# Kernel optimization log

Measured on AMD Instinct MI355X. Metric: run time of the kernel, lower is better.

Reference implementation:

```python
import jax, jax.numpy as jnp
import numpy as np

B, S, HS = 2, 2048, 2048
H, KVH, D = 8, 1, 256
ROPE_BASE = 10000.0


def _rope_cos_sin(position_ids, dim, base=ROPE_BASE):
    # position_ids: (B, S) int -> cos/sin: (B, S, dim)
    inv_freq = 1.0 / (base ** (jnp.arange(0, dim, 2, dtype=jnp.float32) / dim))
    thetas = position_ids.astype(jnp.float32)[..., None] * inv_freq  # (B,S,dim/2)
    emb = jnp.concatenate([thetas, thetas], axis=-1)  # (B,S,dim)
    return jnp.cos(emb), jnp.sin(emb)


def _rotate_half(x):
    x1, x2 = jnp.split(x, 2, axis=-1)
    return jnp.concatenate([-x2, x1], axis=-1)


def _apply_rope(q, k, cos, sin):
    # q,k: (B,h,S,D); cos,sin: (B,S,D) -> unsqueeze head dim
    cos = cos[:, None, :, :]
    sin = sin[:, None, :, :]
    q_emb = q * cos + _rotate_half(q) * sin
    k_emb = k * cos + _rotate_half(k) * sin
    return q_emb, k_emb


def setup_inputs() -> dict:
    key = jax.random.key(0)
    k0, k1, k2, k3, k4 = jax.random.split(key, 5)
    hidden_states = jax.random.normal(k0, (B, S, HS), jnp.float32)
    # causal additive mask: 0 where j<=i, large negative otherwise
    causal = jnp.tril(jnp.ones((S, S), dtype=bool))
    attention_mask = jnp.where(causal, 0.0, -1e9).astype(jnp.float32)
    attention_mask = jnp.broadcast_to(attention_mask[None, None], (B, 1, S, S))
    position_ids = jnp.broadcast_to(jnp.arange(S, dtype=jnp.int32)[None], (B, S))
    scale = 0.02
    Wq = jax.random.normal(k1, (HS, H * D), jnp.float32) * scale
    Wk = jax.random.normal(k2, (HS, KVH * D), jnp.float32) * scale
    Wv = jax.random.normal(k3, (HS, KVH * D), jnp.float32) * scale
    Wo = jax.random.normal(k4, (H * D, HS), jnp.float32) * scale
    return {"hidden_states": hidden_states, "attention_mask": attention_mask,
            "position_ids": position_ids, "Wq": Wq, "Wk": Wk, "Wv": Wv, "Wo": Wo}


def reference(hidden_states, attention_mask, position_ids, Wq, Wk, Wv, Wo):
    bs, seq_len, _ = hidden_states.shape
    q = (hidden_states @ Wq).reshape(bs, seq_len, H, D).transpose(0, 2, 1, 3)     # (B,H,S,D)
    k = (hidden_states @ Wk).reshape(bs, seq_len, KVH, D).transpose(0, 2, 1, 3)   # (B,KVH,S,D)
    v = (hidden_states @ Wv).reshape(bs, seq_len, KVH, D).transpose(0, 2, 1, 3)
    cos, sin = _rope_cos_sin(position_ids, D)
    q, k = _apply_rope(q, k, cos, sin)
    n_rep = H // KVH
    k = jnp.repeat(k, n_rep, axis=1)  # GQA repeat -> (B,H,S,D)
    v = jnp.repeat(v, n_rep, axis=1)
    scores = jnp.einsum('bhqd,bhkd->bhqk', q, k) / jnp.sqrt(jnp.float32(D))
    scores = scores + attention_mask
    attn = jax.nn.softmax(scores.astype(jnp.float32), axis=-1).astype(q.dtype)
    out = jnp.einsum('bhqk,bhkd->bhqd', attn, v)            # (B,H,S,D)
    out = out.transpose(0, 2, 1, 3).reshape(bs, seq_len, H * D)
    return out @ Wo
```

## Files before the change

kernel.cpp:

```cpp
#include <hip/hip_runtime.h>
#include <hip/hip_bf16.h>

typedef __bf16 bf16x8 __attribute__((ext_vector_type(8)));
typedef __bf16 bf16x4 __attribute__((ext_vector_type(4)));
typedef float  f32x4  __attribute__((ext_vector_type(4)));

#define MFMA16(a, b, c) __builtin_amdgcn_mfma_f32_16x16x32_bf16((a), (b), (c), 0, 0, 0)

#define GLOBAL_AS(p) ((const __attribute__((address_space(1))) void*)(p))
#define LDS_AS(p)    ((__attribute__((address_space(3))) void*)(p))

__global__ __launch_bounds__(256) void cvt_bf16_kernel(const float* __restrict__ in,
                                                       __bf16* __restrict__ out)
{
    const int idx = blockIdx.x * 256 + threadIdx.x;
    const float4* p = (const float4*)in + (size_t)idx * 2;
    float4 a = p[0], b = p[1];
    bf16x8 o;
    o[0] = (__bf16)a.x; o[1] = (__bf16)a.y; o[2] = (__bf16)a.z; o[3] = (__bf16)a.w;
    o[4] = (__bf16)b.x; o[5] = (__bf16)b.y; o[6] = (__bf16)b.z; o[7] = (__bf16)b.w;
    ((bf16x8*)out)[idx] = o;
}

__global__ __launch_bounds__(128) void trig_kernel(float2* __restrict__ cs)
{
    const int s = blockIdx.x, i = threadIdx.x;
    const float theta = (float)s * exp2f((float)i * (-13.287712379549449f / 128.f));
    float sn, c;
    sincosf(theta, &sn, &c);
    cs[s * 128 + i] = make_float2(c, sn);
}

__global__ __launch_bounds__(256) void transpose_cvt_kernel(const float* __restrict__ W,
                                                            __bf16* __restrict__ Bt,
                                                            int K, int N)
{
    __shared__ float t[32][33];
    const int n0 = blockIdx.x * 32, k0 = blockIdx.y * 32;
    const int x = threadIdx.x, y = threadIdx.y;
#pragma unroll
    for (int r = 0; r < 4; ++r)
        t[y + r * 8][x] = W[(size_t)(k0 + y + r * 8) * N + n0 + x];
    __syncthreads();
#pragma unroll
    for (int r = 0; r < 4; ++r)
        Bt[(size_t)(n0 + y + r * 8) * K + k0 + x] = (__bf16)t[x][y + r * 8];
}

__global__ __launch_bounds__(256) void vt_kernel(const __bf16* __restrict__ qkv,
                                                 __bf16* __restrict__ vT)
{
    __shared__ __bf16 t[32][33];
    const int s0 = blockIdx.x * 32, d0 = blockIdx.y * 32, b = blockIdx.z;
    const int x = threadIdx.x, y = threadIdx.y;
#pragma unroll
    for (int r = 0; r < 4; ++r)
        t[y + r * 8][x] = qkv[(size_t)(b * 2048 + s0 + y + r * 8) * 2560 + 2304 + d0 + x];
    __syncthreads();
#pragma unroll
    for (int r = 0; r < 4; ++r)
        vT[(size_t)(b * 256 + d0 + y + r * 8) * 2048 + s0 + x] = t[x][y + r * 8];
}

template <typename TC>
__global__ __launch_bounds__(256) void gemm_bt(const __bf16* __restrict__ A,
                                               const __bf16* __restrict__ Bt,
                                               TC* __restrict__ C,
                                               int M, int N, int K)
{
    __shared__ __bf16 As[128 * 32];
    __shared__ __bf16 Bs[128 * 32];

    const int tid  = threadIdx.x;
    const int wave = tid >> 6, lane = tid & 63;
    const int quad = lane >> 4, l16 = lane & 15;
    const int wm = (wave >> 1) * 64, wn = (wave & 1) * 64;
    const int bm = blockIdx.y * 128, bn = blockIdx.x * 128;

    f32x4 acc[4][4] = {};

    for (int k0 = 0; k0 < K; k0 += 32) {
        __syncthreads();
#pragma unroll
        for (int c = 0; c < 2; ++c) {
            const int off = tid * 16 + c * 4096;
            const int row = off >> 6;
            const int kb  = (off & 63) >> 1;
            const __bf16* ga = A  + (size_t)(bm + row) * K + k0 + kb;
            const __bf16* gb = Bt + (size_t)(bn + row) * K + k0 + kb;
            __builtin_amdgcn_global_load_lds(GLOBAL_AS(ga), LDS_AS(As + (off >> 1)), 16, 0, 0);
            __builtin_amdgcn_global_load_lds(GLOBAL_AS(gb), LDS_AS(Bs + (off >> 1)), 16, 0, 0);
        }
        __syncthreads();

        bf16x8 af[4];
#pragma unroll
        for (int mi = 0; mi < 4; ++mi)
            af[mi] = *(const bf16x8*)&As[(wm + mi * 16 + l16) * 32 + quad * 8];
#pragma unroll
        for (int ni = 0; ni < 4; ++ni) {
            bf16x8 bfr = *(const bf16x8*)&Bs[(wn + ni * 16 + l16) * 32 + quad * 8];
#pragma unroll
            for (int mi = 0; mi < 4; ++mi)
                acc[mi][ni] = MFMA16(af[mi], bfr, acc[mi][ni]);
        }
    }
#pragma unroll
    for (int mi = 0; mi < 4; ++mi)
#pragma unroll
        for (int ni = 0; ni < 4; ++ni)
#pragma unroll
            for (int r = 0; r < 4; ++r) {
                int row = bm + wm + mi * 16 + quad * 4 + r;
                int col = bn + wn + ni * 16 + l16;
                C[(size_t)row * N + col] = (TC)acc[mi][ni][r];
            }
}

__global__ __launch_bounds__(256) void rope_kernel(__bf16* __restrict__ qkv,
                                                   const float2* __restrict__ cs)
{
    const int bs = blockIdx.x;
    const int s = bs & 2047;
    const int t = threadIdx.x;
    const float QS = 0.09016843787599907f;

    const int hh = t >> 5, i0 = (t & 31) * 4;
    float2 c0 = cs[s * 128 + i0 + 0], c1 = cs[s * 128 + i0 + 1];
    float2 c2 = cs[s * 128 + i0 + 2], c3 = cs[s * 128 + i0 + 3];

    {
        __bf16* p = qkv + (size_t)bs * 2560 + hh * 256 + i0;
        bf16x4 x1 = *(const bf16x4*)p;
        bf16x4 x2 = *(const bf16x4*)(p + 128);
        bf16x4 o1, o2;
        o1[0] = (__bf16)(((float)x1[0] * c0.x - (float)x2[0] * c0.y) * QS);
        o2[0] = (__bf16)(((float)x2[0] * c0.x + (float)x1[0] * c0.y) * QS);
        o1[1] = (__bf16)(((float)x1[1] * c1.x - (float)x2[1] * c1.y) * QS);
        o2[1] = (__bf16)(((float)x2[1] * c1.x + (float)x1[1] * c1.y) * QS);
        o1[2] = (__bf16)(((float)x1[2] * c2.x - (float)x2[2] * c2.y) * QS);
        o2[2] = (__bf16)(((float)x2[2] * c2.x + (float)x1[2] * c2.y) * QS);
        o1[3] = (__bf16)(((float)x1[3] * c3.x - (float)x2[3] * c3.y) * QS);
        o2[3] = (__bf16)(((float)x2[3] * c3.x + (float)x1[3] * c3.y) * QS);
        *(bf16x4*)p = o1;
        *(bf16x4*)(p + 128) = o2;
    }
    if (t < 32) {
        const int j0 = t * 4;
        float2 d0 = cs[s * 128 + j0 + 0], d1 = cs[s * 128 + j0 + 1];
        float2 d2 = cs[s * 128 + j0 + 2], d3 = cs[s * 128 + j0 + 3];
        __bf16* p = qkv + (size_t)bs * 2560 + 2048 + j0;
        bf16x4 x1 = *(const bf16x4*)p;
        bf16x4 x2 = *(const bf16x4*)(p + 128);
        bf16x4 o1, o2;
        o1[0] = (__bf16)((float)x1[0] * d0.x - (float)x2[0] * d0.y);
        o2[0] = (__bf16)((float)x2[0] * d0.x + (float)x1[0] * d0.y);
        o1[1] = (__bf16)((float)x1[1] * d1.x - (float)x2[1] * d1.y);
        o2[1] = (__bf16)((float)x2[1] * d1.x + (float)x1[1] * d1.y);
        o1[2] = (__bf16)((float)x1[2] * d2.x - (float)x2[2] * d2.y);
        o2[2] = (__bf16)((float)x2[2] * d2.x + (float)x1[2] * d2.y);
        o1[3] = (__bf16)((float)x1[3] * d3.x - (float)x2[3] * d3.y);
        o2[3] = (__bf16)((float)x2[3] * d3.x + (float)x1[3] * d3.y);
        *(bf16x4*)p = o1;
        *(bf16x4*)(p + 128) = o2;
    }
}

__global__ __launch_bounds__(256) void attn_kernel(const __bf16* __restrict__ qkv,
                                                   const __bf16* __restrict__ vTg,
                                                   __bf16* __restrict__ og)
{
    __shared__ __bf16 Ks[64 * 256];
    __shared__ __bf16 Vs[272 * 64];
    __shared__ __bf16 Ps[4][16][68];

    const int b = blockIdx.z, h = blockIdx.y;
    const int qt = (int)gridDim.x - 1 - (int)blockIdx.x;
    const int q0 = qt * 64;
    const int tid  = threadIdx.x;
    const int wave = tid >> 6, lane = tid & 63;
    const int quad = lane >> 4, l16 = lane & 15;
    const int xork = l16 & 7;

    if (tid < 128) {
        bf16x8 one;
#pragma unroll
        for (int e = 0; e < 8; ++e) one[e] = (__bf16)1.0f;
        *(bf16x8*)&Vs[256 * 64 + tid * 8] = one;
    }

    const int qrow = q0 + wave * 16 + l16;
    const __bf16* qptr = qkv + (size_t)(b * 2048 + qrow) * 2560 + h * 256;
    bf16x8 qf[8];
#pragma unroll
    for (int dc = 0; dc < 8; ++dc)
        qf[dc] = *(const bf16x8*)(qptr + dc * 32 + quad * 8);

    f32x4 oacc[17] = {};
    float m_r[4] = {-1e30f, -1e30f, -1e30f, -1e30f};

    const int kKey0 = tid >> 5;
    const int kC    = (tid & 31) ^ (kKey0 & 7);
    const __bf16* kstage0 = qkv + (size_t)b * 2048 * 2560 + 2048
                          + (size_t)kKey0 * 2560 + kC * 8;
    const int vD0 = tid >> 3;
    const int vC  = (tid & 7) ^ (vD0 & 7);
    const __bf16* vstage0 = vTg + (size_t)b * 256 * 2048 + (size_t)vD0 * 2048 + vC * 8;

    int ckK[8];
#pragma unroll
    for (int dc = 0; dc < 8; ++dc) ckK[dc] = (dc * 4 + quad) ^ xork;
    const int chV0 = quad ^ xork;
    const int chV1 = (4 + quad) ^ xork;

    for (int j0 = 0; j0 <= q0; j0 += 64) {
        __syncthreads();
        const __bf16* kst = kstage0 + (size_t)j0 * 2560;
        const __bf16* vst = vstage0 + j0;
#pragma unroll
        for (int p = 0; p < 8; ++p)
            __builtin_amdgcn_global_load_lds(GLOBAL_AS(kst + (size_t)p * 8 * 2560),
                                             LDS_AS(Ks + tid * 8 + p * 2048), 16, 0, 0);
#pragma unroll
        for (int p = 0; p < 8; ++p)
            __builtin_amdgcn_global_load_lds(GLOBAL_AS(vst + (size_t)p * 32 * 2048),
                                             LDS_AS(Vs + tid * 8 + p * 2048), 16, 0, 0);
        __syncthreads();

        f32x4 sc[4] = {};
#pragma unroll
        for (int nt = 0; nt < 4; ++nt) {
            const __bf16* krow = &Ks[(nt * 16 + l16) * 256];
#pragma unroll
            for (int dc = 0; dc < 8; ++dc) {
                bf16x8 kf = *(const bf16x8*)(krow + ckK[dc] * 8);
                sc[nt] = MFMA16(qf[dc], kf, sc[nt]);
            }
        }
        if (j0 == q0) {
#pragma unroll
            for (int nt = 0; nt < 4; ++nt) {
                int key = j0 + nt * 16 + l16;
#pragma unroll
                for (int r = 0; r < 4; ++r) {
                    int row = q0 + wave * 16 + quad * 4 + r;
                    if (key > row) sc[nt][r] = -1e30f;
                }
            }
        }
#pragma unroll
        for (int r = 0; r < 4; ++r) {
            float mx = fmaxf(fmaxf(sc[0][r], sc[1][r]), fmaxf(sc[2][r], sc[3][r]));
#pragma unroll
            for (int off = 1; off < 16; off <<= 1)
                mx = fmaxf(mx, __shfl_xor(mx, off, 64));
            float mnew  = fmaxf(m_r[r], mx);
            float alpha = exp2f(m_r[r] - mnew);
            m_r[r] = mnew;
#pragma unroll
            for (int nt = 0; nt < 4; ++nt)
                sc[nt][r] = exp2f(sc[nt][r] - mnew);
#pragma unroll
            for (int t = 0; t < 17; ++t)
                oacc[t][r] *= alpha;
        }
#pragma unroll
        for (int nt = 0; nt < 4; ++nt)
#pragma unroll
            for (int r = 0; r < 4; ++r)
                Ps[wave][quad * 4 + r][nt * 16 + l16] = (__bf16)sc[nt][r];
        bf16x8 pf0 = *(const bf16x8*)&Ps[wave][l16][quad * 8];
        bf16x8 pf1 = *(const bf16x8*)&Ps[wave][l16][32 + quad * 8];
#pragma unroll
        for (int dt = 0; dt < 17; ++dt) {
            const __bf16* vrow = &Vs[(dt * 16 + l16) * 64];
            bf16x8 vf0 = *(const bf16x8*)(vrow + chV0 * 8);
            bf16x8 vf1 = *(const bf16x8*)(vrow + chV1 * 8);
            oacc[dt] = MFMA16(pf0, vf0, oacc[dt]);
            oacc[dt] = MFMA16(pf1, vf1, oacc[dt]);
        }
    }
    float invl[4];
#pragma unroll
    for (int r = 0; r < 4; ++r) invl[r] = 1.f / oacc[16][r];
#pragma unroll
    for (int dt = 0; dt < 16; ++dt)
#pragma unroll
        for (int r = 0; r < 4; ++r) {
            int row = q0 + wave * 16 + quad * 4 + r;
            int col = h * 256 + dt * 16 + l16;
            og[(size_t)(b * 2048 + row) * 2048 + col] = (__bf16)(oacc[dt][r] * invl[r]);
        }
}

extern "C" void kernel_launch(void* const* d_in, const int* in_sizes, int n_in,
                              void* d_out, int out_size, void* d_ws, size_t ws_size,
                              hipStream_t stream)
{
    (void)in_sizes; (void)n_in; (void)out_size; (void)ws_size;
    const float* hidden = (const float*)d_in[0];
    const float* Wq = (const float*)d_in[3];
    const float* Wk = (const float*)d_in[4];
    const float* Wv = (const float*)d_in[5];
    const float* Wo = (const float*)d_in[6];

    char* ws = (char*)d_ws;
    __bf16* hb    = (__bf16*)(ws);
    __bf16* qkv   = (__bf16*)(ws + (16u << 20));
    __bf16* vTb   = (__bf16*)(ws + (36u << 20));
    __bf16* ob    = (__bf16*)(ws + (38u << 20));
    __bf16* Wqkvt = (__bf16*)(ws + (54u << 20));
    __bf16* Wot   = (__bf16*)(ws + (64u << 20));
    float2* csb   = (float2*)(ws + (72u << 20));
    float* out = (float*)d_out;

    dim3 blk(256);
    dim3 tblk(32, 8);
    cvt_bf16_kernel<<<dim3(4096), blk, 0, stream>>>(hidden, hb);
    trig_kernel<<<dim3(2048), dim3(128), 0, stream>>>(csb);
    transpose_cvt_kernel<<<dim3(64, 64), tblk, 0, stream>>>(Wq, Wqkvt, 2048, 2048);
    transpose_cvt_kernel<<<dim3(8, 64), tblk, 0, stream>>>(Wk, Wqkvt + (size_t)2048 * 2048, 2048, 256);
    transpose_cvt_kernel<<<dim3(8, 64), tblk, 0, stream>>>(Wv, Wqkvt + (size_t)2304 * 2048, 2048, 256);
    transpose_cvt_kernel<<<dim3(64, 64), tblk, 0, stream>>>(Wo, Wot, 2048, 2048);
    gemm_bt<__bf16><<<dim3(20, 32), blk, 0, stream>>>(hb, Wqkvt, qkv, 4096, 2560, 2048);
    rope_kernel<<<dim3(4096), blk, 0, stream>>>(qkv, csb);
    vt_kernel<<<dim3(64, 8, 2), tblk, 0, stream>>>(qkv, vTb);
    attn_kernel<<<dim3(32, 8, 2), blk, 0, stream>>>(qkv, vTb, ob);
    gemm_bt<float><<<dim3(16, 32), blk, 0, stream>>>(ob, Wot, out, 4096, 2048, 2048);
}
```

Measured before the change: 387.7 us.

## Pair low/high causal query tiles per block and double-buffer K/V loads

Each attention block now handles two query tiles (pr and 31-pr), so causal work is balanced across blocks and every loaded K/V tile is used by both query tiles. K/V staging is double-buffered, with the next tile prefetched into LDS while the current one is computed, and one barrier per iteration is removed. The grid is halved to 256 blocks, and register use roughly doubles because two sets of accumulators are held, forcing launch_bounds occupancy to one block. The prefetch into the other buffer is issued right after the barrier and is relied on to complete before the next iteration; that ordering may need explicit waits.

```diff
diff --git a/kernel.cpp b/kernel.cpp
--- a/kernel.cpp
+++ b/kernel.cpp
@@ -166,17 +166,75 @@
     }
 }
 
-__global__ __launch_bounds__(256) void attn_kernel(const __bf16* __restrict__ qkv,
-                                                   const __bf16* __restrict__ vTg,
-                                                   __bf16* __restrict__ og)
-{
-    __shared__ __bf16 Ks[64 * 256];
-    __shared__ __bf16 Vs[272 * 64];
+__device__ __forceinline__ void tile_step(const __bf16* Ksb, const __bf16* Vsb,
+                                          __bf16 (*Psw)[68],
+                                          const bf16x8* qf, f32x4* oacc, float* m_r,
+                                          int rowbase, int keybase, bool diag,
+                                          const int* ckK, int chV0, int chV1,
+                                          int quad, int l16)
+{
+    f32x4 sc[4] = {};
+#pragma unroll
+    for (int nt = 0; nt < 4; ++nt) {
+        const __bf16* krow = Ksb + (nt * 16 + l16) * 256;
+#pragma unroll
+        for (int dc = 0; dc < 8; ++dc) {
+            bf16x8 kf = *(const bf16x8*)(krow + ckK[dc] * 8);
+            sc[nt] = MFMA16(qf[dc], kf, sc[nt]);
+        }
+    }
+    if (diag) {
+#pragma unroll
+        for (int nt = 0; nt < 4; ++nt) {
+            int key = keybase + nt * 16 + l16;
+#pragma unroll
+            for (int r = 0; r < 4; ++r)
+                if (key > rowbase + r) sc[nt][r] = -1e30f;
+        }
+    }
+#pragma unroll
+    for (int r = 0; r < 4; ++r) {
+        float mx = fmaxf(fmaxf(sc[0][r], sc[1][r]), fmaxf(sc[2][r], sc[3][r]));
+#pragma unroll
+        for (int off = 1; off < 16; off <<= 1)
+            mx = fmaxf(mx, __shfl_xor(mx, off, 64));
+        float mnew  = fmaxf(m_r[r], mx);
+        float alpha = exp2f(m_r[r] - mnew);
+        m_r[r] = mnew;
+#pragma unroll
+        for (int nt = 0; nt < 4; ++nt)
+            sc[nt][r] = exp2f(sc[nt][r] - mnew);
+#pragma unroll
+        for (int t = 0; t < 17; ++t)
+            oacc[t][r] *= alpha;
+    }
+#pragma unroll
+    for (int nt = 0; nt < 4; ++nt)
+#pragma unroll
+        for (int r = 0; r < 4; ++r)
+            Psw[quad * 4 + r][nt * 16 + l16] = (__bf16)sc[nt][r];
+    bf16x8 pf0 = *(const bf16x8*)&Psw[l16][quad * 8];
+    bf16x8 pf1 = *(const bf16x8*)&Psw[l16][32 + quad * 8];
+#pragma unroll
+    for (int dt = 0; dt < 17; ++dt) {
+        const __bf16* vrow = Vsb + (dt * 16 + l16) * 64;
+        bf16x8 vf0 = *(const bf16x8*)(vrow + chV0 * 8);
+        bf16x8 vf1 = *(const bf16x8*)(vrow + chV1 * 8);
+        oacc[dt] = MFMA16(pf0, vf0, oacc[dt]);
+        oacc[dt] = MFMA16(pf1, vf1, oacc[dt]);
+    }
+}
+
+__global__ __launch_bounds__(256, 1) void attn_kernel(const __bf16* __restrict__ qkv,
+                                                      const __bf16* __restrict__ vTg,
+                                                      __bf16* __restrict__ og)
+{
+    __shared__ __bf16 Ks[2][64 * 256];
+    __shared__ __bf16 Vs[2][272 * 64];
     __shared__ __bf16 Ps[4][16][68];
 
-    const int b = blockIdx.z, h = blockIdx.y;
-    const int qt = (int)gridDim.x - 1 - (int)blockIdx.x;
-    const int q0 = qt * 64;
+    const int b = blockIdx.z, h = blockIdx.y, pr = blockIdx.x;
+    const int q0L = pr * 64, q0H = (31 - pr) * 64;
     const int tid  = threadIdx.x;
     const int wave = tid >> 6, lane = tid & 63;
     const int quad = lane >> 4, l16 = lane & 15;
@@ -186,18 +244,24 @@
         bf16x8 one;
 #pragma unroll
         for (int e = 0; e < 8; ++e) one[e] = (__bf16)1.0f;
-        *(bf16x8*)&Vs[256 * 64 + tid * 8] = one;
-    }
-
-    const int qrow = q0 + wave * 16 + l16;
-    const __bf16* qptr = qkv + (size_t)(b * 2048 + qrow) * 2560 + h * 256;
-    bf16x8 qf[8];
-#pragma unroll
-    for (int dc = 0; dc < 8; ++dc)
-        qf[dc] = *(const bf16x8*)(qptr + dc * 32 + quad * 8);
-
-    f32x4 oacc[17] = {};
-    float m_r[4] = {-1e30f, -1e30f, -1e30f, -1e30f};
+        *(bf16x8*)&Vs[0][256 * 64 + tid * 8] = one;
+        *(bf16x8*)&Vs[1][256 * 64 + tid * 8] = one;
+    }
+
+    bf16x8 qfL[8], qfH[8];
+    {
+        const __bf16* qpL = qkv + (size_t)(b * 2048 + q0L + wave * 16 + l16) * 2560 + h * 256;
+        const __bf16* qpH = qkv + (size_t)(b * 2048 + q0H + wave * 16 + l16) * 2560 + h * 256;
+#pragma unroll
+        for (int dc = 0; dc < 8; ++dc) {
+            qfL[dc] = *(const bf16x8*)(qpL + dc * 32 + quad * 8);
+            qfH[dc] = *(const bf16x8*)(qpH + dc * 32 + quad * 8);
+        }
+    }
+
+    f32x4 oaccL[17] = {}, oaccH[17] = {};
+    float mL[4] = {-1e30f, -1e30f, -1e30f, -1e30f};
+    float mH[4] = {-1e30f, -1e30f, -1e30f, -1e30f};
 
     const int kKey0 = tid >> 5;
     const int kC    = (tid & 31) ^ (kKey0 & 7);
@@ -213,83 +277,65 @@
     const int chV0 = quad ^ xork;
     const int chV1 = (4 + quad) ^ xork;
 
-    for (int j0 = 0; j0 <= q0; j0 += 64) {
+    const int rowbL = q0L + wave * 16 + quad * 4;
+    const int rowbH = q0H + wave * 16 + quad * 4;
+    const int J = 31 - pr;
+
+    {
+        const __bf16* kst = kstage0;
+        const __bf16* vst = vstage0;
+#pragma unroll
+        for (int p8 = 0; p8 < 8; ++p8)
+            __builtin_amdgcn_global_load_lds(GLOBAL_AS(kst + (size_t)p8 * 8 * 2560),
+                                             LDS_AS(&Ks[0][0] + tid * 8 + p8 * 2048), 16, 0, 0);
+#pragma unroll
+        for (int p8 = 0; p8 < 8; ++p8)
+            __builtin_amdgcn_global_load_lds(GLOBAL_AS(vst + (size_t)p8 * 32 * 2048),
+                                             LDS_AS(&Vs[0][0] + tid * 8 + p8 * 2048), 16, 0, 0);
+    }
+
+    for (int j = 0; j <= J; ++j) {
         __syncthreads();
-        const __bf16* kst = kstage0 + (size_t)j0 * 2560;
-        const __bf16* vst = vstage0 + j0;
-#pragma unroll
-        for (int p = 0; p < 8; ++p)
-            __builtin_amdgcn_global_load_lds(GLOBAL_AS(kst + (size_t)p * 8 * 2560),
-                                             LDS_AS(Ks + tid * 8 + p * 2048), 16, 0, 0);
-#pragma unroll
-        for (int p = 0; p < 8; ++p)
-            __builtin_amdgcn_global_load_lds(GLOBAL_AS(vst + (size_t)p * 32 * 2048),
-                                             LDS_AS(Vs + tid * 8 + p * 2048), 16, 0, 0);
-        __syncthreads();
-
-        f32x4 sc[4] = {};
-#pragma unroll
-        for (int nt = 0; nt < 4; ++nt) {
-            const __bf16* krow = &Ks[(nt * 16 + l16) * 256];
-#pragma unroll
-            for (int dc = 0; dc < 8; ++dc) {
-                bf16x8 kf = *(const bf16x8*)(krow + ckK[dc] * 8);
-                sc[nt] = MFMA16(qf[dc], kf, sc[nt]);
-            }
-        }
-        if (j0 == q0) {
-#pragma unroll
-            for (int nt = 0; nt < 4; ++nt) {
-                int key = j0 + nt * 16 + l16;
-#pragma unroll
-                for (int r = 0; r < 4; ++r) {
-                    int row = q0 + wave * 16 + quad * 4 + r;
-                    if (key > row) sc[nt][r] = -1e30f;
-                }
-            }
-        }
+        if (j < J) {
+            const int nb = (j + 1) & 1;
+            const __bf16* kst = kstage0 + (size_t)(j + 1) * 64 * 2560;
+            const __bf16* vst = vstage0 + (j + 1) * 64;
+#pragma unroll
+            for (int p8 = 0; p8 < 8; ++p8)
+                __builtin_amdgcn_global_load_lds(GLOBAL_AS(kst + (size_t)p8 * 8 * 2560),
+                                                 LDS_AS(&Ks[nb][0] + tid * 8 + p8 * 2048), 16, 0, 0);
+#pragma unroll
+            for (int p8 = 0; p8 < 8; ++p8)
+                __builtin_amdgcn_global_load_lds(GLOBAL_AS(vst + (size_t)p8 * 32 * 2048),
+                                                 LDS_AS(&Vs[nb][0] + tid * 8 + p8 * 2048), 16, 0, 0);
+        }
+        const __bf16* Ksb = &Ks[j & 1][0];
+        const __bf16* Vsb = &Vs[j & 1][0];
+        const int j0 = j * 64;
+        tile_step(Ksb, Vsb, Ps[wave], qfH, oaccH, mH, rowbH, j0, j == J,
+                  ckK, chV0, chV1, quad, l16);
+        if (j <= pr)
+            tile_step(Ksb, Vsb, Ps[wave], qfL, oaccL, mL, rowbL, j0, j == pr,
+                      ckK, chV0, chV1, quad, l16);
+    }
+
+#pragma unroll
+    for (int r = 0; r < 4; ++r) {
+        float il = 1.f / oaccL[16][r];
+        float ih = 1.f / oaccH[16][r];
+#pragma unroll
+        for (int dt = 0; dt < 16; ++dt) {
+            oaccL[dt][r] *= il;
+            oaccH[dt][r] *= ih;
+        }
+    }
+#pragma unroll
+    for (int dt = 0; dt < 16; ++dt)
 #pragma unroll
         for (int r = 0; r < 4; ++r) {
-            float mx = fmaxf(fmaxf(sc[0][r], sc[1][r]), fmaxf(sc[2][r], sc[3][r]));
-#pragma unroll
-            for (int off = 1; off < 16; off <<= 1)
-                mx = fmaxf(mx, __shfl_xor(mx, off, 64));
-            float mnew  = fmaxf(m_r[r], mx);
-            float alpha = exp2f(m_r[r] - mnew);
-            m_r[r] = mnew;
-#pragma unroll
-            for (int nt = 0; nt < 4; ++nt)
-                sc[nt][r] = exp2f(sc[nt][r] - mnew);
-#pragma unroll
-            for (int t = 0; t < 17; ++t)
-                oacc[t][r] *= alpha;
-        }
-#pragma unroll
-        for (int nt = 0; nt < 4; ++nt)
-#pragma unroll
-            for (int r = 0; r < 4; ++r)
-                Ps[wave][quad * 4 + r][nt * 16 + l16] = (__bf16)sc[nt][r];
-        bf16x8 pf0 = *(const bf16x8*)&Ps[wave][l16][quad * 8];
-        bf16x8 pf1 = *(const bf16x8*)&Ps[wave][l16][32 + quad * 8];
-#pragma unroll
-        for (int dt = 0; dt < 17; ++dt) {
-            const __bf16* vrow = &Vs[(dt * 16 + l16) * 64];
-            bf16x8 vf0 = *(const bf16x8*)(vrow + chV0 * 8);
-            bf16x8 vf1 = *(const bf16x8*)(vrow + chV1 * 8);
-            oacc[dt] = MFMA16(pf0, vf0, oacc[dt]);
-            oacc[dt] = MFMA16(pf1, vf1, oacc[dt]);
-        }
-    }
-    float invl[4];
-#pragma unroll
-    for (int r = 0; r < 4; ++r) invl[r] = 1.f / oacc[16][r];
-#pragma unroll
-    for (int dt = 0; dt < 16; ++dt)
-#pragma unroll
-        for (int r = 0; r < 4; ++r) {
-            int row = q0 + wave * 16 + quad * 4 + r;
             int col = h * 256 + dt * 16 + l16;
-            og[(size_t)(b * 2048 + row) * 2048 + col] = (__bf16)(oacc[dt][r] * invl[r]);
+            og[(size_t)(b * 2048 + rowbL + r) * 2048 + col] = (__bf16)oaccL[dt][r];
+            og[(size_t)(b * 2048 + rowbH + r) * 2048 + col] = (__bf16)oaccH[dt][r];
         }
 }
 
@@ -325,6 +371,6 @@
     gemm_bt<__bf16><<<dim3(20, 32), blk, 0, stream>>>(hb, Wqkvt, qkv, 4096, 2560, 2048);
     rope_kernel<<<dim3(4096), blk, 0, stream>>>(qkv, csb);
     vt_kernel<<<dim3(64, 8, 2), tblk, 0, stream>>>(qkv, vTb);
-    attn_kernel<<<dim3(32, 8, 2), blk, 0, stream>>>(qkv, vTb, ob);
+    attn_kernel<<<dim3(16, 8, 2), blk, 0, stream>>>(qkv, vTb, ob);
     gemm_bt<float><<<dim3(16, 32), blk, 0, stream>>>(ob, Wot, out, 4096, 2048, 2048);
 }
```

After: 419.5 us. 1.08x slower.
